# Kernel tuning notes

Measured on AMD Instinct MI355X. Metric: run time of the kernel, lower is better.

The kernel has to match this reference:

```python
import jax, jax.numpy as jnp
import numpy as np

MG = (5, 5)          # mesh_grid_size
UP = (17, 17)        # upsample_size
IMG = (512.0, 512.0) # image_size
B = 8192
FC_OUT = MG[0] * MG[1] * 2  # 50
KH = (UP[0] - 1) // (MG[0] - 1) + 1  # 5
KW = (UP[1] - 1) // (MG[1] - 1) + 1  # 5
SH = (UP[0] - 1) // (MG[0] - 1)      # 4
SW = (UP[1] - 1) // (MG[1] - 1)      # 4
L0 = MG[0] - 1
L1 = MG[1] - 1


def _grid(h, w):
    # channel 0: x coords vary along rows (image_size[0]); channel 1: y along cols
    x_t = jnp.broadcast_to(jnp.linspace(0.0, IMG[0], h)[:, None], (h, w))
    y_t = jnp.broadcast_to(jnp.linspace(0.0, IMG[1], w)[None, :], (h, w))
    return jnp.stack([x_t, y_t], 0)  # [2, h, w]


def _unfold22(a):
    # a: [B, 2, H, W] -> [B, (H-1)*(W-1), 4, 2]; 4 = kernel positions row-major, 2 = channel
    p = jnp.stack([a[:, :, :-1, :-1], a[:, :, :-1, 1:],
                   a[:, :, 1:, :-1], a[:, :, 1:, 1:]], axis=2)  # [B,2,4,H-1,W-1]
    return p.reshape(a.shape[0], 2, 4, -1).transpose(0, 3, 2, 1)


def _persp(src, dst):
    # exact 4-point homography solve (torchgeometry.get_perspective_transform)
    x0, y0 = src[..., 0], src[..., 1]
    u, v = dst[..., 0], dst[..., 1]
    z = jnp.zeros_like(x0)
    o = jnp.ones_like(x0)
    ax = jnp.stack([x0, y0, o, z, z, z, -u * x0, -u * y0], -1)  # [N,4,8]
    ay = jnp.stack([z, z, z, x0, y0, o, -v * x0, -v * y0], -1)
    A = jnp.concatenate([ax, ay], 1)                 # [N,8,8]
    bb = jnp.concatenate([u, v], 1)[..., None]       # [N,8,1]
    h = jnp.linalg.solve(A, bb)[..., 0]              # [N,8]
    return jnp.concatenate([h, o[:, :1]], 1).reshape(-1, 3, 3)


def setup_inputs() -> dict:
    key = jax.random.key(0)
    ks = jax.random.split(key, 4)
    def lin(k, i, o):
        return jax.random.normal(k, (i, o), jnp.float32) / jnp.sqrt(i)
    return {
        "x": jax.random.normal(ks[0], (B, 1024), jnp.float32),
        "W1": lin(ks[1], 1024, 1024), "b1": jnp.zeros((1024,), jnp.float32),
        "W2": lin(ks[2], 1024, 2048), "b2": jnp.zeros((2048,), jnp.float32),
        "W3": lin(ks[3], 2048, FC_OUT), "b3": jnp.zeros((FC_OUT,), jnp.float32),
    }


def reference(x, W1, b1, W2, b2, W3, b3):
    Bn = x.shape[0]
    h = jax.nn.relu(x @ W1 + b1)
    h = jax.nn.relu(h @ W2 + b2)
    out = (h @ W3 + b3).reshape(Bn, 2, MG[0], MG[1])  # [B,2,5,5] mesh flow

    # sparse control grid and 2x2 patch corner points
    gs = _grid(MG[0], MG[1])
    src = _unfold22(jnp.broadcast_to(gs[None], (Bn, 2, MG[0], MG[1]))).reshape(-1, 4, 2)
    flow = _unfold22(out).reshape(-1, 4, 2)
    M = _persp(src, src + flow)  # [B*16, 3, 3]

    # dense grid and its unfold2 (kernel KHxKW, stride SHxSW) patch points
    gd = _grid(UP[0], UP[1])  # [2, 17, 17]
    gi = (np.arange(L0) * SH)[:, None, None, None] + np.arange(KH)[None, None, :, None]
    gj = (np.arange(L1) * SW)[None, :, None, None] + np.arange(KW)[None, None, None, :]
    I, J = np.broadcast_arrays(gi, gj)  # [L0,L1,KH,KW]
    pts = gd[:, I, J].transpose(1, 2, 3, 4, 0).reshape(1, L0 * L1, KH * KW, 2)
    pts = jnp.broadcast_to(pts, (Bn, L0 * L1, KH * KW, 2)).reshape(Bn * L0 * L1, KH * KW, 2)

    # transform_points: homogeneous warp + perspective divide
    ph = jnp.concatenate([pts, jnp.ones(pts.shape[:-1] + (1,), pts.dtype)], -1)
    oh = jnp.einsum('nij,npj->npi', M, ph)
    warped = oh[..., :2] / oh[..., 2:3]
    warped = warped.reshape(Bn, L0, L1, KH, KW, 2)

    # Fold: scatter-accumulate overlapping patches
    fold = jnp.zeros((Bn, 2, UP[0], UP[1]), x.dtype)
    for i in range(L0):
        for j in range(L1):
            blk = warped[:, i, j].transpose(0, 3, 1, 2)  # [B,2,KH,KW]
            fold = fold.at[:, :, i * SH:i * SH + KH, j * SW:j * SW + KW].add(blk)

    # boundary rescaling exactly as the torch code: only the 5x5 crossing points
    idx = np.arange(0, UP[0], MG[0] - 1)
    X, Y = np.meshgrid(idx, idx, indexing='xy')
    fold = fold.at[:, :, X, Y].multiply(0.5)
    for (a, b) in ((0, 0), (0, UP[1] - 1), (UP[0] - 1, UP[1] - 1), (UP[0] - 1, 0)):
        fold = fold.at[:, :, a, b].multiply(2.0)

    return fold - gd[None]  # upsampled mesh flow [B,2,17,17]
```

## Files before the change

### kernel.cpp

```cpp
#include <hip/hip_runtime.h>

typedef __bf16 bf16x8 __attribute__((ext_vector_type(8)));
typedef float f32x4 __attribute__((ext_vector_type(4)));

__device__ __forceinline__ unsigned short f2bf(float f) {
  unsigned int u = __builtin_bit_cast(unsigned int, f);
  unsigned int r = (u + 0x7fffu + ((u >> 16) & 1u)) >> 16;
  return (unsigned short)r;
}

__device__ __forceinline__ float bf2f(unsigned short u) {
  unsigned int v = ((unsigned int)u) << 16;
  return __builtin_bit_cast(float, v);
}

__device__ __forceinline__ void load16_lds(const unsigned short* g, unsigned short* l) {
  __builtin_amdgcn_global_load_lds(
      (const __attribute__((address_space(1))) void*)g,
      (__attribute__((address_space(3))) void*)l, 16, 0, 0);
}

__device__ __forceinline__ void wait_vm0() {
  asm volatile("s_waitcnt vmcnt(0)" ::: "memory");
  __builtin_amdgcn_sched_barrier(0);
}
__device__ __forceinline__ void wait_vm6() {
  asm volatile("s_waitcnt vmcnt(6)" ::: "memory");
  __builtin_amdgcn_sched_barrier(0);
}
__device__ __forceinline__ void wait_vm8() {
  asm volatile("s_waitcnt vmcnt(8)" ::: "memory");
  __builtin_amdgcn_sched_barrier(0);
}
__device__ __forceinline__ void wait_lgkm0() {
  asm volatile("s_waitcnt lgkmcnt(0)" ::: "memory");
  __builtin_amdgcn_sched_barrier(0);
}
__device__ __forceinline__ void barrier_raw() {
  __builtin_amdgcn_sched_barrier(0);
  __builtin_amdgcn_s_barrier();
  __builtin_amdgcn_sched_barrier(0);
}


__global__ __launch_bounds__(256) void prepass(
    const float* __restrict__ x, const float* __restrict__ W1,
    const float* __restrict__ W2, const float* __restrict__ W3,
    unsigned short* __restrict__ xbf, unsigned short* __restrict__ w1t,
    unsigned short* __restrict__ w2t, unsigned short* __restrict__ w3t) {
  __shared__ float tile[32][33];
  const int bid = blockIdx.x;
  const int t = threadIdx.x;
  if (bid < 2048) {
    for (int i = bid * 256 + t; i < 2097152; i += 2048 * 256) {
      float4 f = ((const float4*)x)[i];
      uint2 o;
      o.x = (unsigned)f2bf(f.x) | ((unsigned)f2bf(f.y) << 16);
      o.y = (unsigned)f2bf(f.z) | ((unsigned)f2bf(f.w) << 16);
      ((uint2*)xbf)[i] = o;
    }
  } else if (bid < 3072) {
    int ti = bid - 2048;
    int n0 = (ti & 31) * 32, k0 = (ti >> 5) * 32;
    int tx = t & 31, ty = t >> 5;
    #pragma unroll
    for (int r = 0; r < 32; r += 8)
      tile[ty + r][tx] = W1[(size_t)(k0 + ty + r) * 1024 + n0 + tx];
    __syncthreads();
    #pragma unroll
    for (int r = 0; r < 32; r += 8)
      w1t[(size_t)(n0 + ty + r) * 1024 + k0 + tx] = f2bf(tile[tx][ty + r]);
  } else if (bid < 5120) {
    int ti = bid - 3072;
    int n0 = (ti & 63) * 32, k0 = (ti >> 6) * 32;
    int tx = t & 31, ty = t >> 5;
    #pragma unroll
    for (int r = 0; r < 32; r += 8)
      tile[ty + r][tx] = W2[(size_t)(k0 + ty + r) * 2048 + n0 + tx];
    __syncthreads();
    #pragma unroll
    for (int r = 0; r < 32; r += 8)
      w2t[(size_t)(n0 + ty + r) * 1024 + k0 + tx] = f2bf(tile[tx][ty + r]);
  } else {
    int idx = (bid - 5120) * 256 + t;
    int n = idx >> 11, k = idx & 2047;
    w3t[idx] = f2bf((n < 50) ? W3[(size_t)k * 50 + n] : 0.f);
  }
}


__global__ __launch_bounds__(512, 2) void gemm1_8p(
    const unsigned short* __restrict__ A,
    const unsigned short* __restrict__ Bt,
    const float* __restrict__ bias,
    unsigned short* __restrict__ C) {
  constexpr int K = 1024, N = 1024, NT = 16;
  constexpr int AEL = 256 * 64;
  constexpr int BEL = 128 * 64;
  constexpr int BUF = AEL + BEL;
  __shared__ __align__(16) unsigned short smem[2 * BUF];
  const int t = threadIdx.x;
  const int m0 = blockIdx.x * 256;
  const int n0 = blockIdx.y * 128;
  const int lane = t & 63, wv = t >> 6;
  const int l16 = lane & 15, quad = lane >> 4;
  const int wr = wv >> 1, wc = wv & 1;
  const int rb = wr * 64, cb = wc * 64;

  const int srow = t >> 3;
  const int sg = ((t & 7) ^ (srow & 7)) * 8;
  const unsigned short* Ag0 = A + (size_t)(m0 + srow) * K + sg;
  const unsigned short* Bg0 = Bt + (size_t)(n0 + srow) * K + sg;
  const int ldsO = wv * 8 * 64;

  f32x4 acc[4][4] = {};

  #pragma unroll
  for (int r = 0; r < 4; ++r)
    load16_lds(Ag0 + (size_t)(r * 64) * K, &smem[r * 4096 + ldsO]);
  #pragma unroll
  for (int r = 0; r < 2; ++r)
    load16_lds(Bg0 + (size_t)(r * 64) * K, &smem[AEL + r * 4096 + ldsO]);

  for (int kt = 0; kt < NT; ++kt) {
    unsigned short* Ls = &smem[(kt & 1) * BUF];

    if (kt + 1 < NT) {
      unsigned short* Ln = &smem[((kt + 1) & 1) * BUF];
      const unsigned short* An = Ag0 + (size_t)(kt + 1) * 64;
      const unsigned short* Bn = Bg0 + (size_t)(kt + 1) * 64;
      #pragma unroll
      for (int r = 0; r < 4; ++r)
        load16_lds(An + (size_t)(r * 64) * K, &Ln[r * 4096 + ldsO]);
      #pragma unroll
      for (int r = 0; r < 2; ++r)
        load16_lds(Bn + (size_t)(r * 64) * K, &Ln[AEL + r * 4096 + ldsO]);
      wait_vm6();
    } else {
      wait_vm0();
    }
    barrier_raw();

    bf16x8 af[4], bfr[4];

    #pragma unroll
    for (int ni = 0; ni < 4; ++ni) {
      int row = cb + ni * 16 + l16;
      bfr[ni] = *(const bf16x8*)&Ls[AEL + row * 64 + (quad ^ (row & 7)) * 8];
    }
    #pragma unroll
    for (int mi = 0; mi < 4; ++mi) {
      int row = rb + mi * 16 + l16;
      af[mi] = *(const bf16x8*)&Ls[row * 64 + (quad ^ (row & 7)) * 8];
    }
    barrier_raw();
    wait_lgkm0();
    __builtin_amdgcn_s_setprio(1);
    #pragma unroll
    for (int mi = 0; mi < 4; ++mi)
      #pragma unroll
      for (int ni = 0; ni < 4; ++ni)
        acc[mi][ni] = __builtin_amdgcn_mfma_f32_16x16x32_bf16(
            af[mi], bfr[ni], acc[mi][ni], 0, 0, 0);
    __builtin_amdgcn_s_setprio(0);
    barrier_raw();

    #pragma unroll
    for (int ni = 0; ni < 4; ++ni) {
      int row = cb + ni * 16 + l16;
      bfr[ni] = *(const bf16x8*)&Ls[AEL + row * 64 + ((4 + quad) ^ (row & 7)) * 8];
    }
    #pragma unroll
    for (int mi = 0; mi < 4; ++mi) {
      int row = rb + mi * 16 + l16;
      af[mi] = *(const bf16x8*)&Ls[row * 64 + ((4 + quad) ^ (row & 7)) * 8];
    }
    barrier_raw();
    wait_lgkm0();
    __builtin_amdgcn_s_setprio(1);
    #pragma unroll
    for (int mi = 0; mi < 4; ++mi)
      #pragma unroll
      for (int ni = 0; ni < 4; ++ni)
        acc[mi][ni] = __builtin_amdgcn_mfma_f32_16x16x32_bf16(
            af[mi], bfr[ni], acc[mi][ni], 0, 0, 0);
    __builtin_amdgcn_s_setprio(0);
    barrier_raw();
  }

  unsigned short* Cs = smem;
  float bv[4];
  #pragma unroll
  for (int ni = 0; ni < 4; ++ni) bv[ni] = bias[n0 + cb + ni * 16 + l16];
  #pragma unroll
  for (int mi = 0; mi < 4; ++mi)
    #pragma unroll
    for (int ni = 0; ni < 4; ++ni)
      #pragma unroll
      for (int r = 0; r < 4; ++r) {
        int row = rb + mi * 16 + quad * 4 + r;
        int col = cb + ni * 16 + l16;
        int pb = (col >> 3) ^ (row & 15);
        Cs[row * 128 + pb * 8 + (col & 7)] = f2bf(fmaxf(acc[mi][ni][r] + bv[ni], 0.f));
      }
  __syncthreads();
  #pragma unroll
  for (int j = 0; j < 8; ++j) {
    int idx = j * 512 + t;
    int row = idx >> 4, cg = idx & 15;
    int pb = cg ^ (row & 15);
    *(uint4*)&C[(size_t)(m0 + row) * N + n0 + cg * 8] =
        *(const uint4*)&Cs[row * 128 + pb * 8];
  }
}


__global__ __launch_bounds__(512, 2) void gemm2_8p(
    const unsigned short* __restrict__ A,
    const unsigned short* __restrict__ Bt,
    const float* __restrict__ bias,
    const unsigned short* __restrict__ W3t,
    unsigned short* __restrict__ part) {
  constexpr int K = 1024, NT = 16;
  constexpr int AEL = 256 * 64;
  constexpr int BUF = 2 * AEL;
  __shared__ __align__(16) unsigned short smem[2 * BUF];
  const int t = threadIdx.x;
  const int m0 = blockIdx.x * 256;
  const int n0 = blockIdx.y * 256;
  const int lane = t & 63, wv = t >> 6;
  const int l16 = lane & 15, quad = lane >> 4;
  const int wr = wv >> 2, wc = wv & 3;
  const int rb = wr * 128, cb = wc * 64;

  const int srow = t >> 3;
  const int sg = ((t & 7) ^ (srow & 7)) * 8;
  const unsigned short* Ag0 = A + (size_t)(m0 + srow) * K + sg;
  const unsigned short* Bg0 = Bt + (size_t)(n0 + srow) * K + sg;
  const int ldsO = wv * 8 * 64;

  f32x4 acc[8][4] = {};

  #pragma unroll
  for (int r = 0; r < 4; ++r) {
    load16_lds(Ag0 + (size_t)(r * 64) * K, &smem[r * 4096 + ldsO]);
    load16_lds(Bg0 + (size_t)(r * 64) * K, &smem[AEL + r * 4096 + ldsO]);
  }

  for (int kt = 0; kt < NT; ++kt) {
    unsigned short* Ls = &smem[(kt & 1) * BUF];

    if (kt + 1 < NT) {
      unsigned short* Ln = &smem[((kt + 1) & 1) * BUF];
      const unsigned short* An = Ag0 + (size_t)(kt + 1) * 64;
      const unsigned short* Bn = Bg0 + (size_t)(kt + 1) * 64;
      #pragma unroll
      for (int r = 0; r < 4; ++r) {
        load16_lds(An + (size_t)(r * 64) * K, &Ln[r * 4096 + ldsO]);
        load16_lds(Bn + (size_t)(r * 64) * K, &Ln[AEL + r * 4096 + ldsO]);
      }
      wait_vm8();
    } else {
      wait_vm0();
    }
    barrier_raw();

    bf16x8 af[4], bfr[4];

    #pragma unroll
    for (int ni = 0; ni < 4; ++ni) {
      int row = cb + ni * 16 + l16;
      bfr[ni] = *(const bf16x8*)&Ls[AEL + row * 64 + (quad ^ (row & 7)) * 8];
    }
    #pragma unroll
    for (int mi = 0; mi < 4; ++mi) {
      int row = rb + mi * 16 + l16;
      af[mi] = *(const bf16x8*)&Ls[row * 64 + (quad ^ (row & 7)) * 8];
    }
    barrier_raw();
    wait_lgkm0();
    __builtin_amdgcn_s_setprio(1);
    #pragma unroll
    for (int mi = 0; mi < 4; ++mi)
      #pragma unroll
      for (int ni = 0; ni < 4; ++ni)
        acc[mi][ni] = __builtin_amdgcn_mfma_f32_16x16x32_bf16(
            af[mi], bfr[ni], acc[mi][ni], 0, 0, 0);
    __builtin_amdgcn_s_setprio(0);
    barrier_raw();

    #pragma unroll
    for (int mi = 0; mi < 4; ++mi) {
      int row = rb + 64 + mi * 16 + l16;
      af[mi] = *(const bf16x8*)&Ls[row * 64 + (quad ^ (row & 7)) * 8];
    }
    barrier_raw();
    wait_lgkm0();
    __builtin_amdgcn_s_setprio(1);
    #pragma unroll
    for (int mi = 0; mi < 4; ++mi)
      #pragma unroll
      for (int ni = 0; ni < 4; ++ni)
        acc[4 + mi][ni] = __builtin_amdgcn_mfma_f32_16x16x32_bf16(
            af[mi], bfr[ni], acc[4 + mi][ni], 0, 0, 0);
    __builtin_amdgcn_s_setprio(0);
    barrier_raw();

    #pragma unroll
    for (int ni = 0; ni < 4; ++ni) {
      int row = cb + ni * 16 + l16;
      bfr[ni] = *(const bf16x8*)&Ls[AEL + row * 64 + ((4 + quad) ^ (row & 7)) * 8];
    }
    #pragma unroll
    for (int mi = 0; mi < 4; ++mi) {
      int row = rb + 64 + mi * 16 + l16;
      af[mi] = *(const bf16x8*)&Ls[row * 64 + ((4 + quad) ^ (row & 7)) * 8];
    }
    barrier_raw();
    wait_lgkm0();
    __builtin_amdgcn_s_setprio(1);
    #pragma unroll
    for (int mi = 0; mi < 4; ++mi)
      #pragma unroll
      for (int ni = 0; ni < 4; ++ni)
        acc[4 + mi][ni] = __builtin_amdgcn_mfma_f32_16x16x32_bf16(
            af[mi], bfr[ni], acc[4 + mi][ni], 0, 0, 0);
    __builtin_amdgcn_s_setprio(0);
    barrier_raw();

    #pragma unroll
    for (int mi = 0; mi < 4; ++mi) {
      int row = rb + mi * 16 + l16;
      af[mi] = *(const bf16x8*)&Ls[row * 64 + ((4 + quad) ^ (row & 7)) * 8];
    }
    barrier_raw();
    wait_lgkm0();
    __builtin_amdgcn_s_setprio(1);
    #pragma unroll
    for (int mi = 0; mi < 4; ++mi)
      #pragma unroll
      for (int ni = 0; ni < 4; ++ni)
        acc[mi][ni] = __builtin_amdgcn_mfma_f32_16x16x32_bf16(
            af[mi], bfr[ni], acc[mi][ni], 0, 0, 0);
    __builtin_amdgcn_s_setprio(0);
    barrier_raw();
  }

  unsigned short* Cs = smem;
  float bv[4];
  #pragma unroll
  for (int ni = 0; ni < 4; ++ni) bv[ni] = bias[n0 + cb + ni * 16 + l16];
  #pragma unroll
  for (int mi = 0; mi < 8; ++mi)
    #pragma unroll
    for (int ni = 0; ni < 4; ++ni)
      #pragma unroll
      for (int r = 0; r < 4; ++r) {
        int row = rb + mi * 16 + quad * 4 + r;
        int col = cb + ni * 16 + l16;
        int pb = (col >> 3) ^ (row & 31);
        Cs[row * 256 + pb * 8 + (col & 7)] = f2bf(fmaxf(acc[mi][ni][r] + bv[ni], 0.f));
      }
  __syncthreads();

  bf16x8 bq[8][4];
  #pragma unroll
  for (int ks = 0; ks < 8; ++ks)
    #pragma unroll
    for (int nt = 0; nt < 4; ++nt)
      bq[ks][nt] = *(const bf16x8*)&W3t[(size_t)(nt * 16 + l16) * 2048 +
                                        n0 + ks * 32 + quad * 8];
  f32x4 acc2[2][4] = {};
  #pragma unroll
  for (int ks = 0; ks < 8; ++ks) {
    bf16x8 af2[2];
    #pragma unroll
    for (int mt = 0; mt < 2; ++mt) {
      int row = wv * 32 + mt * 16 + l16;
      int pb = (ks * 4 + quad) ^ (row & 31);
      af2[mt] = *(const bf16x8*)&Cs[row * 256 + pb * 8];
    }
    #pragma unroll
    for (int mt = 0; mt < 2; ++mt)
      #pragma unroll
      for (int nt = 0; nt < 4; ++nt)
        acc2[mt][nt] = __builtin_amdgcn_mfma_f32_16x16x32_bf16(
            af2[mt], bq[ks][nt], acc2[mt][nt], 0, 0, 0);
  }

  unsigned short* pp = part + (size_t)blockIdx.y * 8192 * 64;
  #pragma unroll
  for (int mt = 0; mt < 2; ++mt)
    #pragma unroll
    for (int nt = 0; nt < 4; ++nt) {
      int col = nt * 16 + l16;
      #pragma unroll
      for (int r = 0; r < 4; ++r) {
        int row = m0 + wv * 32 + mt * 16 + quad * 4 + r;
        pp[(size_t)row * 64 + col] = f2bf(acc2[mt][nt][r]);
      }
    }
}


__global__ __launch_bounds__(256) void geom_reduce(
    const unsigned short* __restrict__ part, const float* __restrict__ b3,
    float* __restrict__ outp) {
  __shared__ float s_out3[16 * 64];
  __shared__ float fold[16 * 578];
  const int t = threadIdx.x;
  const int bbase = blockIdx.x * 16;

  for (int i = t; i < 16 * 578; i += 256) fold[i] = 0.f;
  for (int i = t; i < 1024; i += 256) {
    int m = i >> 6, n = i & 63;
    size_t idx = (size_t)(bbase + m) * 64 + n;
    float v = 0.f;
    #pragma unroll
    for (int z = 0; z < 8; ++z) v += bf2f(part[idx + (size_t)z * 8192 * 64]);
    s_out3[i] = v + ((n < 50) ? b3[n] : 0.f);
  }
  __syncthreads();

  {
    const int bl = t >> 4;
    const int p = t & 15;
    const int pi = p >> 2, pj = p & 3;
    const float* o = &s_out3[bl * 64];

    float u00 = 128.f * pi       + o[pi * 5 + pj];
    float v00 = 128.f * pj       + o[25 + pi * 5 + pj];
    float u01 = 128.f * pi       + o[pi * 5 + pj + 1];
    float v01 = 128.f * (pj + 1) + o[25 + pi * 5 + pj + 1];
    float u10 = 128.f * (pi + 1) + o[(pi + 1) * 5 + pj];
    float v10 = 128.f * pj       + o[25 + (pi + 1) * 5 + pj];
    float u11 = 128.f * (pi + 1) + o[(pi + 1) * 5 + pj + 1];
    float v11 = 128.f * (pj + 1) + o[25 + (pi + 1) * 5 + pj + 1];

    float sx = u00 - u10 + u11 - u01;
    float sy = v00 - v10 + v11 - v01;
    float dx1 = u10 - u11, dx2 = u01 - u11;
    float dy1 = v10 - v11, dy2 = v01 - v11;
    float rden = 1.f / (dx1 * dy2 - dx2 * dy1);
    float g = (sx * dy2 - dx2 * sy) * rden;
    float h = (dx1 * sy - sx * dy1) * rden;
    float a = u10 - u00 + g * u10;
    float b = u01 - u00 + h * u01;
    float c = u00;
    float d = v10 - v00 + g * v10;
    float e = v01 - v00 + h * v01;
    float f = v00;

    #pragma unroll
    for (int ai = 0; ai < 5; ++ai) {
      #pragma unroll
      for (int bi = 0; bi < 5; ++bi) {
        float s = 0.25f * ai, tt = 0.25f * bi;
        float rw = 1.f / (g * s + h * tt + 1.f);
        float xx = (a * s + b * tt + c) * rw;
        float yy = (d * s + e * tt + f) * rw;
        int gi = pi * 4 + ai, gj = pj * 4 + bi;
        atomicAdd(&fold[(bl * 2 + 0) * 289 + gi * 17 + gj], xx);
        atomicAdd(&fold[(bl * 2 + 1) * 289 + gi * 17 + gj], yy);
      }
    }
  }
  __syncthreads();

  for (int i = t; i < 16 * 578; i += 256) {
    int blb = i / 578;
    int rem = i - blb * 578;
    int ch = rem / 289;
    int ij = rem - ch * 289;
    int gi = ij / 17, gj = ij - gi * 17;
    float val = fold[i];
    if ((gi % 4 == 0) && (gj % 4 == 0)) val *= 0.5f;
    if ((gi == 0 || gi == 16) && (gj == 0 || gj == 16)) val *= 2.f;
    val -= (ch == 0) ? 32.f * gi : 32.f * gj;
    outp[(size_t)(bbase + blb) * 578 + rem] = val;
  }
}


extern "C" void kernel_launch(void* const* d_in, const int* in_sizes, int n_in,
                              void* d_out, int out_size, void* d_ws, size_t ws_size,
                              hipStream_t stream) {
  const float* x  = (const float*)d_in[0];
  const float* W1 = (const float*)d_in[1];
  const float* b1 = (const float*)d_in[2];
  const float* W2 = (const float*)d_in[3];
  const float* b2 = (const float*)d_in[4];
  const float* W3 = (const float*)d_in[5];
  const float* b3 = (const float*)d_in[6];
  float* outp = (float*)d_out;

  char* ws = (char*)d_ws;
  unsigned short* xbf = (unsigned short*)ws;
  unsigned short* w1t = (unsigned short*)(ws + (size_t)16 * 1024 * 1024);
  unsigned short* part = (unsigned short*)ws;
  unsigned short* w2t = (unsigned short*)(ws + (size_t)34 * 1024 * 1024);
  unsigned short* w3t = (unsigned short*)(ws + (size_t)38 * 1024 * 1024);
  unsigned short* h1  = (unsigned short*)(ws + (size_t)38 * 1024 * 1024 + 512 * 1024);

  prepass<<<5632, 256, 0, stream>>>(x, W1, W2, W3, xbf, w1t, w2t, w3t);

  gemm1_8p<<<dim3(32, 8), 512, 0, stream>>>(xbf, w1t, b1, h1);
  gemm2_8p<<<dim3(32, 8), 512, 0, stream>>>(h1, w2t, b2, w3t, part);
  geom_reduce<<<512, 256, 0, stream>>>(part, b3, outp);
}
```

Before: 204.5 us.

## Simplify GEMM main loops to one barrier per k-tile and compiler-scheduled LDS reads

Replaces the hand-scheduled ping-pong loops in both GEMM kernels with a simpler scheme. Each k-tile now waits for all outstanding global-to-LDS loads and takes one barrier, then issues the next tile's prefetch and runs two unrolled halves of LDS fragment reads and MFMAs. The manual lgkm waits, s_setprio hints and the several barriers per iteration are gone, which should cut synchronisation overhead and let the compiler interleave LDS reads with MFMAs. The trade-off is that vmcnt(0) at the top of each iteration waits for the previous prefetch rather than allowing partial overlap, and the larger kernel holds more fragment registers live at once.

```diff
diff --git a/kernel.cpp b/kernel.cpp
--- a/kernel.cpp
+++ b/kernel.cpp
@@ -22,18 +22,6 @@
 
 __device__ __forceinline__ void wait_vm0() {
   asm volatile("s_waitcnt vmcnt(0)" ::: "memory");
-  __builtin_amdgcn_sched_barrier(0);
-}
-__device__ __forceinline__ void wait_vm6() {
-  asm volatile("s_waitcnt vmcnt(6)" ::: "memory");
-  __builtin_amdgcn_sched_barrier(0);
-}
-__device__ __forceinline__ void wait_vm8() {
-  asm volatile("s_waitcnt vmcnt(8)" ::: "memory");
-  __builtin_amdgcn_sched_barrier(0);
-}
-__device__ __forceinline__ void wait_lgkm0() {
-  asm volatile("s_waitcnt lgkmcnt(0)" ::: "memory");
   __builtin_amdgcn_sched_barrier(0);
 }
 __device__ __forceinline__ void barrier_raw() {
@@ -125,6 +113,9 @@
   for (int kt = 0; kt < NT; ++kt) {
     unsigned short* Ls = &smem[(kt & 1) * BUF];
 
+    wait_vm0();
+    barrier_raw();
+
     if (kt + 1 < NT) {
       unsigned short* Ln = &smem[((kt + 1) & 1) * BUF];
       const unsigned short* An = Ag0 + (size_t)(kt + 1) * 64;
@@ -135,58 +126,30 @@
       #pragma unroll
       for (int r = 0; r < 2; ++r)
         load16_lds(Bn + (size_t)(r * 64) * K, &Ln[AEL + r * 4096 + ldsO]);
-      wait_vm6();
-    } else {
-      wait_vm0();
-    }
-    barrier_raw();
-
-    bf16x8 af[4], bfr[4];
-
-    #pragma unroll
-    for (int ni = 0; ni < 4; ++ni) {
-      int row = cb + ni * 16 + l16;
-      bfr[ni] = *(const bf16x8*)&Ls[AEL + row * 64 + (quad ^ (row & 7)) * 8];
-    }
-    #pragma unroll
-    for (int mi = 0; mi < 4; ++mi) {
-      int row = rb + mi * 16 + l16;
-      af[mi] = *(const bf16x8*)&Ls[row * 64 + (quad ^ (row & 7)) * 8];
-    }
-    barrier_raw();
-    wait_lgkm0();
-    __builtin_amdgcn_s_setprio(1);
-    #pragma unroll
-    for (int mi = 0; mi < 4; ++mi)
-      #pragma unroll
-      for (int ni = 0; ni < 4; ++ni)
-        acc[mi][ni] = __builtin_amdgcn_mfma_f32_16x16x32_bf16(
-            af[mi], bfr[ni], acc[mi][ni], 0, 0, 0);
-    __builtin_amdgcn_s_setprio(0);
-    barrier_raw();
-
-    #pragma unroll
-    for (int ni = 0; ni < 4; ++ni) {
-      int row = cb + ni * 16 + l16;
-      bfr[ni] = *(const bf16x8*)&Ls[AEL + row * 64 + ((4 + quad) ^ (row & 7)) * 8];
-    }
-    #pragma unroll
-    for (int mi = 0; mi < 4; ++mi) {
-      int row = rb + mi * 16 + l16;
-      af[mi] = *(const bf16x8*)&Ls[row * 64 + ((4 + quad) ^ (row & 7)) * 8];
-    }
-    barrier_raw();
-    wait_lgkm0();
-    __builtin_amdgcn_s_setprio(1);
-    #pragma unroll
-    for (int mi = 0; mi < 4; ++mi)
-      #pragma unroll
-      for (int ni = 0; ni < 4; ++ni)
-        acc[mi][ni] = __builtin_amdgcn_mfma_f32_16x16x32_bf16(
-            af[mi], bfr[ni], acc[mi][ni], 0, 0, 0);
-    __builtin_amdgcn_s_setprio(0);
-    barrier_raw();
-  }
+    }
+
+    #pragma unroll
+    for (int half = 0; half < 2; ++half) {
+      bf16x8 af[4], bfr[4];
+      #pragma unroll
+      for (int ni = 0; ni < 4; ++ni) {
+        int row = cb + ni * 16 + l16;
+        bfr[ni] = *(const bf16x8*)&Ls[AEL + row * 64 + ((half * 4 + quad) ^ (row & 7)) * 8];
+      }
+      #pragma unroll
+      for (int mi = 0; mi < 4; ++mi) {
+        int row = rb + mi * 16 + l16;
+        af[mi] = *(const bf16x8*)&Ls[row * 64 + ((half * 4 + quad) ^ (row & 7)) * 8];
+      }
+      #pragma unroll
+      for (int mi = 0; mi < 4; ++mi)
+        #pragma unroll
+        for (int ni = 0; ni < 4; ++ni)
+          acc[mi][ni] = __builtin_amdgcn_mfma_f32_16x16x32_bf16(
+              af[mi], bfr[ni], acc[mi][ni], 0, 0, 0);
+    }
+  }
+  barrier_raw();
 
   unsigned short* Cs = smem;
   float bv[4];
@@ -250,6 +213,9 @@
   for (int kt = 0; kt < NT; ++kt) {
     unsigned short* Ls = &smem[(kt & 1) * BUF];
 
+    wait_vm0();
+    barrier_raw();
+
     if (kt + 1 < NT) {
       unsigned short* Ln = &smem[((kt + 1) & 1) * BUF];
       const unsigned short* An = Ag0 + (size_t)(kt + 1) * 64;
@@ -259,92 +225,31 @@
         load16_lds(An + (size_t)(r * 64) * K, &Ln[r * 4096 + ldsO]);
         load16_lds(Bn + (size_t)(r * 64) * K, &Ln[AEL + r * 4096 + ldsO]);
       }
-      wait_vm8();
-    } else {
-      wait_vm0();
-    }
-    barrier_raw();
-
-    bf16x8 af[4], bfr[4];
-
-    #pragma unroll
-    for (int ni = 0; ni < 4; ++ni) {
-      int row = cb + ni * 16 + l16;
-      bfr[ni] = *(const bf16x8*)&Ls[AEL + row * 64 + (quad ^ (row & 7)) * 8];
-    }
-    #pragma unroll
-    for (int mi = 0; mi < 4; ++mi) {
-      int row = rb + mi * 16 + l16;
-      af[mi] = *(const bf16x8*)&Ls[row * 64 + (quad ^ (row & 7)) * 8];
-    }
-    barrier_raw();
-    wait_lgkm0();
-    __builtin_amdgcn_s_setprio(1);
-    #pragma unroll
-    for (int mi = 0; mi < 4; ++mi)
-      #pragma unroll
-      for (int ni = 0; ni < 4; ++ni)
-        acc[mi][ni] = __builtin_amdgcn_mfma_f32_16x16x32_bf16(
-            af[mi], bfr[ni], acc[mi][ni], 0, 0, 0);
-    __builtin_amdgcn_s_setprio(0);
-    barrier_raw();
-
-    #pragma unroll
-    for (int mi = 0; mi < 4; ++mi) {
-      int row = rb + 64 + mi * 16 + l16;
-      af[mi] = *(const bf16x8*)&Ls[row * 64 + (quad ^ (row & 7)) * 8];
-    }
-    barrier_raw();
-    wait_lgkm0();
-    __builtin_amdgcn_s_setprio(1);
-    #pragma unroll
-    for (int mi = 0; mi < 4; ++mi)
-      #pragma unroll
-      for (int ni = 0; ni < 4; ++ni)
-        acc[4 + mi][ni] = __builtin_amdgcn_mfma_f32_16x16x32_bf16(
-            af[mi], bfr[ni], acc[4 + mi][ni], 0, 0, 0);
-    __builtin_amdgcn_s_setprio(0);
-    barrier_raw();
-
-    #pragma unroll
-    for (int ni = 0; ni < 4; ++ni) {
-      int row = cb + ni * 16 + l16;
-      bfr[ni] = *(const bf16x8*)&Ls[AEL + row * 64 + ((4 + quad) ^ (row & 7)) * 8];
-    }
-    #pragma unroll
-    for (int mi = 0; mi < 4; ++mi) {
-      int row = rb + 64 + mi * 16 + l16;
-      af[mi] = *(const bf16x8*)&Ls[row * 64 + ((4 + quad) ^ (row & 7)) * 8];
-    }
-    barrier_raw();
-    wait_lgkm0();
-    __builtin_amdgcn_s_setprio(1);
-    #pragma unroll
-    for (int mi = 0; mi < 4; ++mi)
-      #pragma unroll
-      for (int ni = 0; ni < 4; ++ni)
-        acc[4 + mi][ni] = __builtin_amdgcn_mfma_f32_16x16x32_bf16(
-            af[mi], bfr[ni], acc[4 + mi][ni], 0, 0, 0);
-    __builtin_amdgcn_s_setprio(0);
-    barrier_raw();
-
-    #pragma unroll
-    for (int mi = 0; mi < 4; ++mi) {
-      int row = rb + mi * 16 + l16;
-      af[mi] = *(const bf16x8*)&Ls[row * 64 + ((4 + quad) ^ (row & 7)) * 8];
-    }
-    barrier_raw();
-    wait_lgkm0();
-    __builtin_amdgcn_s_setprio(1);
-    #pragma unroll
-    for (int mi = 0; mi < 4; ++mi)
-      #pragma unroll
-      for (int ni = 0; ni < 4; ++ni)
-        acc[mi][ni] = __builtin_amdgcn_mfma_f32_16x16x32_bf16(
-            af[mi], bfr[ni], acc[mi][ni], 0, 0, 0);
-    __builtin_amdgcn_s_setprio(0);
-    barrier_raw();
-  }
+    }
+
+    #pragma unroll
+    for (int half = 0; half < 2; ++half) {
+      bf16x8 bfr[4];
+      #pragma unroll
+      for (int ni = 0; ni < 4; ++ni) {
+        int row = cb + ni * 16 + l16;
+        bfr[ni] = *(const bf16x8*)&Ls[AEL + row * 64 + ((half * 4 + quad) ^ (row & 7)) * 8];
+      }
+      bf16x8 af[8];
+      #pragma unroll
+      for (int mi = 0; mi < 8; ++mi) {
+        int row = rb + mi * 16 + l16;
+        af[mi] = *(const bf16x8*)&Ls[row * 64 + ((half * 4 + quad) ^ (row & 7)) * 8];
+      }
+      #pragma unroll
+      for (int mi = 0; mi < 8; ++mi)
+        #pragma unroll
+        for (int ni = 0; ni < 4; ++ni)
+          acc[mi][ni] = __builtin_amdgcn_mfma_f32_16x16x32_bf16(
+              af[mi], bfr[ni], acc[mi][ni], 0, 0, 0);
+    }
+  }
+  barrier_raw();
 
   unsigned short* Cs = smem;
   float bv[4];
```

Result: faster. 200.3 us (-2.0%).
